# Optimization experiments

Hardware: AMD Instinct MI355X
Metric: run time of the kernel (lower is better)

The kernel has to match this reference:

```python
import jax, jax.numpy as jnp
import numpy as np

B, S, D_MODEL = 2, 2048, 2048
N_HEADS, N_KV_HEADS, HEAD_DIM = 32, 8, 64
N_GROUPS = N_HEADS // N_KV_HEADS


def setup_inputs() -> dict:
    key = jax.random.key(0)
    ks = jax.random.split(key, 5)
    x = jax.random.normal(ks[0], (B, S, D_MODEL), dtype=jnp.float32)
    wq = jax.random.normal(ks[1], (N_HEADS * HEAD_DIM, D_MODEL), dtype=jnp.float32) * 0.02
    wk = jax.random.normal(ks[2], (N_KV_HEADS * HEAD_DIM, D_MODEL), dtype=jnp.float32) * 0.02
    wv = jax.random.normal(ks[3], (N_KV_HEADS * HEAD_DIM, D_MODEL), dtype=jnp.float32) * 0.02
    wo = jax.random.normal(ks[4], (D_MODEL, N_HEADS * HEAD_DIM), dtype=jnp.float32) * 0.02
    # Rotary tables: module's apply_rope expects cos/sin of shape [S, head_dim//2]
    half = HEAD_DIM // 2
    inv_freq = 1.0 / (10000.0 ** (jnp.arange(0, half, dtype=jnp.float32) / half))
    angles = jnp.arange(S, dtype=jnp.float32)[:, None] * inv_freq[None, :]  # [S, half]
    cos = jnp.cos(angles)
    sin = jnp.sin(angles)
    return {"x": x, "wq": wq, "wk": wk, "wv": wv, "wo": wo, "cos": cos, "sin": sin}


def _rotate_half(t):
    half = t.shape[-1] // 2
    return jnp.concatenate((-t[..., half:], t[..., :half]), axis=-1)


def _apply_rope(q, k, cos, sin):
    # cos/sin: [S, head_dim//2] -> repeat_interleave(2) -> [S, head_dim]
    cos2 = jnp.repeat(cos, 2, axis=-1)[None, :, None, :]  # [1,S,1,D]
    sin2 = jnp.repeat(sin, 2, axis=-1)[None, :, None, :]
    q_rot = q * cos2 + _rotate_half(q) * sin2
    k_rot = k * cos2 + _rotate_half(k) * sin2
    return q_rot, k_rot


def reference(x, wq, wk, wv, wo, cos, sin):
    b, s, _ = x.shape
    q = (x @ wq.T).reshape(b, s, N_HEADS, HEAD_DIM)
    k = (x @ wk.T).reshape(b, s, N_KV_HEADS, HEAD_DIM)
    v = (x @ wv.T).reshape(b, s, N_KV_HEADS, HEAD_DIM)
    q, k = _apply_rope(q, k, cos, sin)
    # GQA expansion: repeat_interleave along head dim
    k = jnp.repeat(k, N_GROUPS, axis=2)  # [b,s,H,D]
    v = jnp.repeat(v, N_GROUPS, axis=2)
    q = q.transpose(0, 2, 1, 3)  # [b,H,s,D]
    k = k.transpose(0, 2, 1, 3)
    v = v.transpose(0, 2, 1, 3)
    scale = HEAD_DIM ** -0.5
    scores = jnp.einsum("bhqd,bhkd->bhqk", q, k) * scale
    causal = jnp.tril(jnp.ones((s, s), dtype=bool))
    scores = jnp.where(causal[None, None], scores, jnp.finfo(scores.dtype).min)
    attn = jax.nn.softmax(scores, axis=-1)
    out = jnp.einsum("bhqk,bhkd->bhqd", attn, v)
    out = out.transpose(0, 2, 1, 3).reshape(b, s, N_HEADS * HEAD_DIM)
    return out @ wo.T
```

## Files before the change

kernel.cpp:

```cpp
#include <hip/hip_runtime.h>
#include <hip/hip_bf16.h>

#define B_   2
#define S_   2048
#define DM   2048
#define NH   32
#define NKV  8
#define HD   64
#define MROWS 4096
#define NQKV  3072

typedef __attribute__((ext_vector_type(8))) short bf16x8;
typedef __attribute__((ext_vector_type(4))) float f32x4;
typedef __attribute__((ext_vector_type(16))) float f32x16;

__device__ __forceinline__ unsigned short f2b(float f) {
  __hip_bfloat16 h = __float2bfloat16(f);
  return *reinterpret_cast<unsigned short*>(&h);
}

__device__ __forceinline__ void gload16(const void* g, void* l) {
  __builtin_amdgcn_global_load_lds((__attribute__((address_space(1))) void*)g,
                                   (__attribute__((address_space(3))) void*)l,
                                   16, 0, 0);
// ... 87 lines not shown
  };
  auto ldB = [&](int buf, int row, int c16) -> bf16x8 {
    return *(const bf16x8*)((const char*)&Bbuf[buf][0] + row * 128 + ((c16 ^ (row & 7)) << 4));
  };

  f32x4 acc[4][4];
#pragma unroll
  for (int a = 0; a < 4; a++)
#pragma unroll
    for (int b2 = 0; b2 < 4; b2++) acc[a][b2] = (f32x4){0.f, 0.f, 0.f, 0.f};

  const int l15 = lane & 15, l4 = lane >> 4;

  stage_half(0, 0, 0); stage_half(0, 0, 1);
  stage_half(1, 64, 0); stage_half(1, 64, 1);
  asm volatile("s_waitcnt vmcnt(6)" ::: "memory");
  __builtin_amdgcn_s_barrier();

  int cur = 0;
  for (int t = 0; t < NT; ++t) {
    const int nxt2 = (cur >= 1) ? cur - 1 : cur + 2;
    {
      bf16x8 af[4], bfv[4];
#pragma unroll
      for (int mt = 0; mt < 4; ++mt) af[mt] = ldA(cur, wr * 64 + mt * 16 + l15, l4);
#pragma unroll
      for (int nt = 0; nt < 4; ++nt) bfv[nt] = ldB(cur, wc * 64 + nt * 16 + l15, l4);
      if (t + 2 < NT) stage_half(nxt2, (t + 2) * 64, 0);
      __builtin_amdgcn_s_barrier();
      __builtin_amdgcn_s_setprio(1);
#pragma unroll
      for (int mt = 0; mt < 4; ++mt)
#pragma unroll
        for (int nt = 0; nt < 4; ++nt)
          acc[mt][nt] = __builtin_amdgcn_mfma_f32_16x16x32_bf16(af[mt], bfv[nt], acc[mt][nt], 0, 0, 0);
      __builtin_amdgcn_s_setprio(0);
      __builtin_amdgcn_s_barrier();
    }
    {
      bf16x8 af[4], bfv[4];
#pragma unroll
      for (int mt = 0; mt < 4; ++mt) af[mt] = ldA(cur, wr * 64 + mt * 16 + l15, 4 + l4);
#pragma unroll
      for (int nt = 0; nt < 4; ++nt) bfv[nt] = ldB(cur, wc * 64 + nt * 16 + l15, 4 + l4);
      if (t + 2 < NT) stage_half(nxt2, (t + 2) * 64, 1);
      __builtin_amdgcn_s_barrier();
      __builtin_amdgcn_s_setprio(1);
#pragma unroll
      for (int mt = 0; mt < 4; ++mt)
#pragma unroll
        for (int nt = 0; nt < 4; ++nt)
          acc[mt][nt] = __builtin_amdgcn_mfma_f32_16x16x32_bf16(af[mt], bfv[nt], acc[mt][nt], 0, 0, 0);
      __builtin_amdgcn_s_setprio(0);
      if (t < NT - 1) {
        if (t + 2 < NT) asm volatile("s_waitcnt vmcnt(6)" ::: "memory");
        else            asm volatile("s_waitcnt vmcnt(0)" ::: "memory");
        __builtin_amdgcn_s_barrier();
      }
    }
    cur = (cur < 2) ? cur + 1 : 0;
  }

  const int orow = rowbase + wr * 64, ocol = colbase + wc * 64;
#pragma unroll
  for (int mt = 0; mt < 4; ++mt)
#pragma unroll
    for (int r = 0; r < 4; ++r) {
      const int row = orow + mt * 16 + l4 * 4 + r;
      const int s = row & 2047;
      const float* cR = cosg + s * 32;
      const float* sR = sing + s * 32;
#pragma unroll
      for (int nt = 0; nt < 2; ++nt) {
        const int i2 = nt * 8 + (l15 >> 1);
        float c0 = cR[i2], sv0 = sR[i2], c1 = cR[16 + i2], sv1 = sR[16 + i2];
        float alo = acc[mt][nt][r], ahi = acc[mt][nt + 2][r];
        size_t base = (size_t)row * 2048 + ocol + nt * 16 + l15;
        Qb[base]      = f2b((alo * c0 - ahi * sv0) * QSCALE);
        Qb[base + 32] = f2b((ahi * c1 + alo * sv1) * QSCALE);
      }
    }
}

__global__ __launch_bounds__(256, 3) void gemm_kv(const unsigned short* __restrict__ A,
                                                  const unsigned short* __restrict__ Bm,
                                                  unsigned short* __restrict__ Kb2,
                                                  unsigned short* __restrict__ Vtb,
                                                  const float* __restrict__ cosg,
                                                  const float* __restrict__ sing) {
  const int K = DM;
  __shared__ unsigned short Abuf[3][128 * 32];
  __shared__ unsigned short Bbuf[3][128 * 32];
  const int tid = threadIdx.x;
  const int wave = tid >> 6, lane = tid & 63;
  const int wr = wave >> 1, wc = wave & 1;
  const int rowbase = blockIdx.y * 128;
  const int colbase = blockIdx.x * 128;
  const unsigned short* Ag = A + (size_t)rowbase * K;
  const unsigned short* Bg = Bm + (size_t)colbase * K;
  const int NT = K / 32;

  auto stage = [&](int buf, int k0) {
#pragma unroll
    for (int it = 0; it < 2; ++it) {
      int slot = wave * 128 + it * 64 + lane;
      int r = slot >> 2, p = slot & 3;
      gload16(Ag + (size_t)r * K + k0 + ((p ^ ((r >> 1) & 3)) << 3),
              &Abuf[buf][(wave * 128 + it * 64) * 8]);
    }
#pragma unroll
    for (int it = 0; it < 2; ++it) {
      int slot = wave * 128 + it * 64 + lane;
      int r = slot >> 2, p = slot & 3;
      gload16(Bg + (size_t)r * K + k0 + ((p ^ ((r >> 1) & 3)) << 3),
              &Bbuf[buf][(wave * 128 + it * 64) * 8]);
    }
  };
  auto ldA = [&](int buf, int row, int c) -> bf16x8 {
    return *(const bf16x8*)((const char*)&Abuf[buf][0] + row * 64 + ((c ^ ((row >> 1) & 3)) << 4));
  };
  auto ldB = [&](int buf, int row, int c) -> bf16x8 {
    return *(const bf16x8*)((const char*)&Bbuf[buf][0] + row * 64 + ((c ^ ((row >> 1) & 3)) << 4));
  };

  f32x4 acc[4][4];
#pragma unroll
  for (int a = 0; a < 4; a++)
#pragma unroll
    for (int b2 = 0; b2 < 4; b2++) acc[a][b2] = (f32x4){0.f, 0.f, 0.f, 0.f};

  const int l15 = lane & 15, l4 = lane >> 4;

  stage(0, 0);
  stage(1, 32);
  asm volatile("s_waitcnt vmcnt(4)" ::: "memory");
  __builtin_amdgcn_s_barrier();

  int cur = 0;
  for (int t = 0; t < NT; ++t) {
    const int nxt2 = (cur >= 1) ? cur - 1 : cur + 2;
    bf16x8 af[4], bfv[4];
#pragma unroll
    for (int mt = 0; mt < 4; ++mt) af[mt] = ldA(cur, wr * 64 + mt * 16 + l15, l4);
#pragma unroll
    for (int nt = 0; nt < 4; ++nt) bfv[nt] = ldB(cur, wc * 64 + nt * 16 + l15, l4);
    if (t + 2 < NT) stage(nxt2, (t + 2) * 32);
    __builtin_amdgcn_s_barrier();
    __builtin_amdgcn_s_setprio(1);
#pragma unroll
    for (int mt = 0; mt < 4; ++mt)
#pragma unroll
      for (int nt = 0; nt < 4; ++nt)
        acc[mt][nt] = __builtin_amdgcn_mfma_f32_16x16x32_bf16(af[mt], bfv[nt], acc[mt][nt], 0, 0, 0);
    __builtin_amdgcn_s_setprio(0);
    if (t < NT - 1) {
      if (t + 2 < NT) asm volatile("s_waitcnt vmcnt(4)" ::: "memory");
      else            asm volatile("s_waitcnt vmcnt(0)" ::: "memory");
      __builtin_amdgcn_s_barrier();
    }
    cur = (cur < 2) ? cur + 1 : 0;
  }

  const int orow = rowbase + wr * 64, ocol = colbase + wc * 64;
  if (colbase < 512) {
#pragma unroll
    for (int mt = 0; mt < 4; ++mt)
#pragma unroll
      for (int r = 0; r < 4; ++r) {
        const int row = orow + mt * 16 + l4 * 4 + r;
        const int s = row & 2047;
        const float* cR = cosg + s * 32;
        const float* sR = sing + s * 32;
#pragma unroll
        for (int nt = 0; nt < 2; ++nt) {
          const int i2 = nt * 8 + (l15 >> 1);
          float c0 = cR[i2], sv0 = sR[i2], c1 = cR[16 + i2], sv1 = sR[16 + i2];
          float alo = acc[mt][nt][r], ahi = acc[mt][nt + 2][r];
          size_t base = (size_t)row * 512 + ocol + nt * 16 + l15;
          Kb2[base]      = f2b(alo * c0 - ahi * sv0);
          Kb2[base + 32] = f2b(ahi * c1 + alo * sv1);
        }
      }
  } else {
    const int hkv = (ocol - 512) >> 6;
#pragma unroll
    for (int mt = 0; mt < 4; ++mt)
#pragma unroll
      for (int nt = 0; nt < 4; ++nt) {
        const int d = nt * 16 + l15;
        const int row0 = orow + mt * 16 + l4 * 4;
        const int b = row0 >> 11, s0i = row0 & 2047;
        ushort4 u;
        u.x = f2b(acc[mt][nt][0]); u.y = f2b(acc[mt][nt][1]);
        u.z = f2b(acc[mt][nt][2]); u.w = f2b(acc[mt][nt][3]);
        *(ushort4*)(Vtb + ((size_t)(b * NKV + hkv) * HD + d) * S_ + s0i) = u;
      }
  }
}

#define BMg 256
#define BNg 128
#define BKg 64
__global__ __launch_bounds__(512, 2) void gemm_bt(const unsigned short* __restrict__ A,
                                                  const unsigned short* __restrict__ Bm,
                                                  float* __restrict__ C,
                                                  int M, int N, int K) {
  __shared__ unsigned short Abuf[3][BMg * BKg];
  __shared__ unsigned short Bbuf[3][BNg * BKg];
  const int tid = threadIdx.x;
  const int wave = tid >> 6, lane = tid & 63;
  const int wr = wave >> 1, wc = wave & 1;
  const int rowbase = blockIdx.y * BMg;
  const int colbase = blockIdx.x * BNg;
  const unsigned short* Ag = A + (size_t)rowbase * K;
  const unsigned short* Bg = Bm + (size_t)colbase * K;
  const int NT = K / BKg;

  auto stage_half = [&](int buf, int k0, int half) {
#pragma unroll
    for (int i = 0; i < 2; ++i) {
      int c = wave * 256 + (half * 2 + i) * 64 + lane;
      int r = c >> 3, p = c & 7;
      gload16(Ag + (size_t)r * K + k0 + ((p ^ (r & 7)) << 3),
              &Abuf[buf][(wave * 256 + (half * 2 + i) * 64) * 8]);
    }
    int c = wave * 128 + half * 64 + lane;
    int r = c >> 3, p = c & 7;
    gload16(Bg + (size_t)r * K + k0 + ((p ^ (r & 7)) << 3),
            &Bbuf[buf][(wave * 128 + half * 64) * 8]);
  };
  auto ldA = [&](int buf, int row, int c16) -> bf16x8 {
    return *(const bf16x8*)((const char*)&Abuf[buf][0] + row * 128 + ((c16 ^ (row & 7)) << 4));
  };
  auto ldB = [&](int buf, int row, int c16) -> bf16x8 {
    return *(const bf16x8*)((const char*)&Bbuf[buf][0] + row * 128 + ((c16 ^ (row & 7)) << 4));
  };

  f32x4 acc[4][4];
#pragma unroll
  for (int a = 0; a < 4; a++)
#pragma unroll
    for (int b2 = 0; b2 < 4; b2++) acc[a][b2] = (f32x4){0.f, 0.f, 0.f, 0.f};

  const int l15 = lane & 15, l4 = lane >> 4;

  stage_half(0, 0, 0); stage_half(0, 0, 1);
  stage_half(1, BKg, 0); stage_half(1, BKg, 1);
  asm volatile("s_waitcnt vmcnt(6)" ::: "memory");
  __builtin_amdgcn_s_barrier();

  int cur = 0;
  for (int t = 0; t < NT; ++t) {
    const int nxt2 = (cur >= 1) ? cur - 1 : cur + 2;
    {
      bf16x8 af[4], bfv[4];
#pragma unroll
      for (int mt = 0; mt < 4; ++mt) af[mt] = ldA(cur, wr * 64 + mt * 16 + l15, l4);
#pragma unroll
      for (int nt = 0; nt < 4; ++nt) bfv[nt] = ldB(cur, wc * 64 + nt * 16 + l15, l4);
      if (t + 2 < NT) stage_half(nxt2, (t + 2) * BKg, 0);
      __builtin_amdgcn_s_barrier();
      __builtin_amdgcn_s_setprio(1);
#pragma unroll
      for (int mt = 0; mt < 4; ++mt)
#pragma unroll
        for (int nt = 0; nt < 4; ++nt)
          acc[mt][nt] = __builtin_amdgcn_mfma_f32_16x16x32_bf16(af[mt], bfv[nt], acc[mt][nt], 0, 0, 0);
      __builtin_amdgcn_s_setprio(0);
      __builtin_amdgcn_s_barrier();
    }
    {
      bf16x8 af[4], bfv[4];
#pragma unroll
      for (int mt = 0; mt < 4; ++mt) af[mt] = ldA(cur, wr * 64 + mt * 16 + l15, 4 + l4);
#pragma unroll
      for (int nt = 0; nt < 4; ++nt) bfv[nt] = ldB(cur, wc * 64 + nt * 16 + l15, 4 + l4);
      if (t + 2 < NT) stage_half(nxt2, (t + 2) * BKg, 1);
      __builtin_amdgcn_s_barrier();
      __builtin_amdgcn_s_setprio(1);
#pragma unroll
      for (int mt = 0; mt < 4; ++mt)
#pragma unroll
        for (int nt = 0; nt < 4; ++nt)
          acc[mt][nt] = __builtin_amdgcn_mfma_f32_16x16x32_bf16(af[mt], bfv[nt], acc[mt][nt], 0, 0, 0);
      __builtin_amdgcn_s_setprio(0);
      if (t < NT - 1) {
        if (t + 2 < NT) asm volatile("s_waitcnt vmcnt(6)" ::: "memory");
        else            asm volatile("s_waitcnt vmcnt(0)" ::: "memory");
        __builtin_amdgcn_s_barrier();
      }
    }
    cur = (cur < 2) ? cur + 1 : 0;
  }

  const int orow = rowbase + wr * 64, ocol = colbase + wc * 64;
#pragma unroll
  for (int mt = 0; mt < 4; mt++)
#pragma unroll
    for (int nt = 0; nt < 4; nt++)
#pragma unroll
      for (int r = 0; r < 4; r++)
        C[(size_t)(orow + mt * 16 + l4 * 4 + r) * N + ocol + nt * 16 + l15] = acc[mt][nt][r];
}

__global__ __launch_bounds__(256, 2) void attn_kernel(const unsigned short* __restrict__ Qb,
                                                      const unsigned short* __restrict__ Kb2,
                                                      const unsigned short* __restrict__ Vt,
                                                      unsigned short* __restrict__ AO) {
  const int pr = blockIdx.x, h = blockIdx.y, b = blockIdx.z;
  const int hk = h >> 2;
  __shared__ unsigned short Kbuf[2][8192];
  __shared__ unsigned short Vbuf[2][8192];
  const int tid = threadIdx.x, wave = tid >> 6, lane = tid & 63;
  const int l31 = lane & 31, hi = lane >> 5;

  const unsigned short* Qrow = Qb + (size_t)b * S_ * 2048 + h * 64;
  const unsigned short* Krow = Kb2 + (size_t)b * S_ * 512 + hk * 64;
  const unsigned short* Vbase = Vt + (size_t)(b * NKV + hk) * HD * S_;

  const int NT_A = 16 - pr;
  const int NTtot = 17;

  auto j0_of = [&](int tl) { return (tl < NT_A ? tl : tl - NT_A) * 128; };
  auto stage = [&](int j0, int bufi) {
#pragma unroll
    for (int it = 0; it < 4; ++it) {
      int slot = (wave * 4 + it) * 64 + lane;
      int row = slot >> 3, p = slot & 7;
      gload16(Krow + (size_t)(j0 + row) * 512 + ((p ^ (row & 7)) << 3),
              &Kbuf[bufi][(wave * 4 + it) * 512]);
    }
#pragma unroll
    for (int it = 0; it < 4; ++it) {
      int slot = (wave * 4 + it) * 64 + lane;
      int row = slot >> 4, p = slot & 15;
      gload16(Vbase + (size_t)row * S_ + j0 + ((p ^ (row & 15)) << 3),
              &Vbuf[bufi][(wave * 4 + it) * 512]);
    }
  };

  stage(j0_of(0), 0);
  stage(j0_of(1), 1);
  asm volatile("s_waitcnt vmcnt(8)" ::: "memory");
  __builtin_amdgcn_s_barrier();

  int cur = 0, tlin = 0;

  for (int rg = 0; rg < 2; ++rg) {
    const int qbi = rg == 0 ? (15 - pr) : pr;
    const int qb = qbi * 128;
    const int NT = qbi + 1;
    const int q0w = qb + wave * 32;
    const int qg = q0w + l31;

    bf16x8 qf[4];
#pragma unroll
    for (int c = 0; c < 4; ++c)
      qf[c] = *reinterpret_cast<const bf16x8*>(Qrow + (size_t)qg * 2048 + c * 16 + hi * 8);

    f32x16 Oa0 = {}, Oa1 = {};
    float m_old = -INFINITY, lsum = 0.f;

    for (int t = 0; t < NT; ++t, ++tlin) {
      const int j0 = t * 128;

      if (j0 < q0w + 32) {
        const char* Klc = (const char*)&Kbuf[cur][0];
        const char* Vlc = (const char*)&Vbuf[cur][0];

        f32x16 s0 = {}, s1 = {}, s2 = {}, s3 = {};
        __builtin_amdgcn_s_setprio(1);
#pragma unroll
        for (int c = 0; c < 4; ++c) {
          const int xb = ((c << 1) + hi) ^ (l31 & 7);
          bf16x8 kf0 = *(const bf16x8*)(Klc + (l31) * 128       + (xb << 4));
          s0 = __builtin_amdgcn_mfma_f32_32x32x16_bf16(kf0, qf[c], s0, 0, 0, 0);
          bf16x8 kf1 = *(const bf16x8*)(Klc + (32 + l31) * 128  + (xb << 4));
          s1 = __builtin_amdgcn_mfma_f32_32x32x16_bf16(kf1, qf[c], s1, 0, 0, 0);
          bf16x8 kf2 = *(const bf16x8*)(Klc + (64 + l31) * 128  + (xb << 4));
          s2 = __builtin_amdgcn_mfma_f32_32x32x16_bf16(kf2, qf[c], s2, 0, 0, 0);
          bf16x8 kf3 = *(const bf16x8*)(Klc + (96 + l31) * 128  + (xb << 4));
          s3 = __builtin_amdgcn_mfma_f32_32x32x16_bf16(kf3, qf[c], s3, 0, 0, 0);
        }
        __builtin_amdgcn_s_setprio(0);

        if (j0 + 127 > q0w) {
          const int kb0 = j0 + 4 * hi, kb1 = kb0 + 32, kb2m = kb0 + 64, kb3 = kb0 + 96;
#pragma unroll
          for (int r = 0; r < 16; ++r) {
            const int ko = (r & 3) + 8 * (r >> 2);
            if (kb0 + ko > qg) s0[r] = -INFINITY;
            if (kb1 + ko > qg) s1[r] = -INFINITY;
            if (kb2m + ko > qg) s2[r] = -INFINITY;
            if (kb3 + ko > qg) s3[r] = -INFINITY;
          }
        }

        float a0 = fmaxf(fmaxf(s0[0], s1[0]), fmaxf(s2[0], s3[0]));
        float a1 = fmaxf(fmaxf(s0[1], s1[1]), fmaxf(s2[1], s3[1]));
        float a2 = fmaxf(fmaxf(s0[2], s1[2]), fmaxf(s2[2], s3[2]));
        float a3 = fmaxf(fmaxf(s0[3], s1[3]), fmaxf(s2[3], s3[3]));
#pragma unroll
        for (int r = 4; r < 16; r += 4) {
          a0 = fmaxf(a0, fmaxf(fmaxf(s0[r], s1[r]), fmaxf(s2[r], s3[r])));
          a1 = fmaxf(a1, fmaxf(fmaxf(s0[r + 1], s1[r + 1]), fmaxf(s2[r + 1], s3[r + 1])));
          a2 = fmaxf(a2, fmaxf(fmaxf(s0[r + 2], s1[r + 2]), fmaxf(s2[r + 2], s3[r + 2])));
          a3 = fmaxf(a3, fmaxf(fmaxf(s0[r + 3], s1[r + 3]), fmaxf(s2[r + 3], s3[r + 3])));
        }
        float mxt = fmaxf(fmaxf(a0, a1), fmaxf(a2, a3));
        mxt = fmaxf(mxt, __shfl_xor(mxt, 32, 64));

        if (!__all(mxt - m_old <= 8.f)) {
          float mnew = fmaxf(m_old, mxt);
          float corr = exp2hw(m_old - mnew);
          m_old = mnew;
          lsum *= corr;
#pragma unroll
          for (int r = 0; r < 16; ++r) { Oa0[r] *= corr; Oa1[r] *= corr; }
        }

        float t0 = 0.f, t1 = 0.f, t2 = 0.f, t3 = 0.f;
#pragma unroll
        for (int r = 0; r < 16; r += 4) {
          s0[r]     = exp2hw(s0[r] - m_old);     t0 += s0[r];
          s0[r + 1] = exp2hw(s0[r + 1] - m_old); t1 += s0[r + 1];
          s0[r + 2] = exp2hw(s0[r + 2] - m_old); t2 += s0[r + 2];
          s0[r + 3] = exp2hw(s0[r + 3] - m_old); t3 += s0[r + 3];
        }
#pragma unroll
        for (int r = 0; r < 16; r += 4) {
          s1[r]     = exp2hw(s1[r] - m_old);     t0 += s1[r];
          s1[r + 1] = exp2hw(s1[r + 1] - m_old); t1 += s1[r + 1];
          s1[r + 2] = exp2hw(s1[r + 2] - m_old); t2 += s1[r + 2];
          s1[r + 3] = exp2hw(s1[r + 3] - m_old); t3 += s1[r + 3];
        }
#pragma unroll
        for (int r = 0; r < 16; r += 4) {
          s2[r]     = exp2hw(s2[r] - m_old);     t0 += s2[r];
          s2[r + 1] = exp2hw(s2[r + 1] - m_old); t1 += s2[r + 1];
          s2[r + 2] = exp2hw(s2[r + 2] - m_old); t2 += s2[r + 2];
          s2[r + 3] = exp2hw(s2[r + 3] - m_old); t3 += s2[r + 3];
        }
#pragma unroll
        for (int r = 0; r < 16; r += 4) {
          s3[r]     = exp2hw(s3[r] - m_old);     t0 += s3[r];
          s3[r + 1] = exp2hw(s3[r + 1] - m_old); t1 += s3[r + 1];
          s3[r + 2] = exp2hw(s3[r + 2] - m_old); t2 += s3[r + 2];
          s3[r + 3] = exp2hw(s3[r + 3] - m_old); t3 += s3[r + 3];
        }
        float rs = (t0 + t1) + (t2 + t3);
        rs += __shfl_xor(rs, 32, 64);
        lsum += rs;

        bf16x8 pf0, pf1, pf2, pf3, pf4, pf5, pf6, pf7;
        {
          unsigned aA = cvtpk(s0[0], s0[1]),  bA = cvtpk(s0[4], s0[5]);  pl32swap(aA, bA);
          unsigned aB = cvtpk(s0[2], s0[3]),  bB = cvtpk(s0[6], s0[7]);  pl32swap(aB, bB);
          pf0 = mk8(aA, aB, bA, bB);
          unsigned aC = cvtpk(s0[8], s0[9]),  bC = cvtpk(s0[12], s0[13]); pl32swap(aC, bC);
          unsigned aD = cvtpk(s0[10], s0[11]), bD = cvtpk(s0[14], s0[15]); pl32swap(aD, bD);
          pf1 = mk8(aC, aD, bC, bD);
        }
        {
          unsigned aA = cvtpk(s1[0], s1[1]),  bA = cvtpk(s1[4], s1[5]);  pl32swap(aA, bA);
          unsigned aB = cvtpk(s1[2], s1[3]),  bB = cvtpk(s1[6], s1[7]);  pl32swap(aB, bB);
          pf2 = mk8(aA, aB, bA, bB);
          unsigned aC = cvtpk(s1[8], s1[9]),  bC = cvtpk(s1[12], s1[13]); pl32swap(aC, bC);
          unsigned aD = cvtpk(s1[10], s1[11]), bD = cvtpk(s1[14], s1[15]); pl32swap(aD, bD);
          pf3 = mk8(aC, aD, bC, bD);
        }
        {
          unsigned aA = cvtpk(s2[0], s2[1]),  bA = cvtpk(s2[4], s2[5]);  pl32swap(aA, bA);
          unsigned aB = cvtpk(s2[2], s2[3]),  bB = cvtpk(s2[6], s2[7]);  pl32swap(aB, bB);
          pf4 = mk8(aA, aB, bA, bB);
          unsigned aC = cvtpk(s2[8], s2[9]),  bC = cvtpk(s2[12], s2[13]); pl32swap(aC, bC);
          unsigned aD = cvtpk(s2[10], s2[11]), bD = cvtpk(s2[14], s2[15]); pl32swap(aD, bD);
          pf5 = mk8(aC, aD, bC, bD);
        }
        {
          unsigned aA = cvtpk(s3[0], s3[1]),  bA = cvtpk(s3[4], s3[5]);  pl32swap(aA, bA);
          unsigned aB = cvtpk(s3[2], s3[3]),  bB = cvtpk(s3[6], s3[7]);  pl32swap(aB, bB);
          pf6 = mk8(aA, aB, bA, bB);
          unsigned aC = cvtpk(s3[8], s3[9]),  bC = cvtpk(s3[12], s3[13]); pl32swap(aC, bC);
          unsigned aD = cvtpk(s3[10], s3[11]), bD = cvtpk(s3[14], s3[15]); pl32swap(aD, bD);
          pf7 = mk8(aC, aD, bC, bD);
        }

        const int xv = l31 & 15;
        __builtin_amdgcn_s_setprio(1);
#define PVSTEP(PF, SK)                                                                     \
        {                                                                                  \
          const int xc = (((SK) << 1) + hi) ^ xv;                                          \
          bf16x8 vf0 = *(const bf16x8*)(Vlc + l31 * 256 + (xc << 4));                      \
          Oa0 = __builtin_amdgcn_mfma_f32_32x32x16_bf16(vf0, PF, Oa0, 0, 0, 0);            \
          bf16x8 vf1 = *(const bf16x8*)(Vlc + (32 + l31) * 256 + (xc << 4));               \
          Oa1 = __builtin_amdgcn_mfma_f32_32x32x16_bf16(vf1, PF, Oa1, 0, 0, 0);            \
        }
        PVSTEP(pf0, 0) PVSTEP(pf1, 1) PVSTEP(pf2, 2) PVSTEP(pf3, 3)
        PVSTEP(pf4, 4) PVSTEP(pf5, 5) PVSTEP(pf6, 6) PVSTEP(pf7, 7)
#undef PVSTEP
        __builtin_amdgcn_s_setprio(0);
      }

      __builtin_amdgcn_s_barrier();
      if (tlin + 2 < NTtot) stage(j0_of(tlin + 2), cur);
      if (tlin + 1 < NTtot) {
        if (tlin + 2 < NTtot) asm volatile("s_waitcnt vmcnt(8)" ::: "memory");
        else                  asm volatile("s_waitcnt vmcnt(0)" ::: "memory");
        __builtin_amdgcn_s_barrier();
      }
      cur ^= 1;
    }

    const float inv = 1.0f / lsum;
    unsigned short* ob = AO + (size_t)(b * S_ + qg) * 2048 + h * 64;
#pragma unroll
    for (int c = 0; c < 4; ++c) {
      ushort4 u0, u1;
      u0.x = f2b(Oa0[4 * c] * inv);     u0.y = f2b(Oa0[4 * c + 1] * inv);
      u0.z = f2b(Oa0[4 * c + 2] * inv); u0.w = f2b(Oa0[4 * c + 3] * inv);
      u1.x = f2b(Oa1[4 * c] * inv);     u1.y = f2b(Oa1[4 * c + 1] * inv);
      u1.z = f2b(Oa1[4 * c + 2] * inv); u1.w = f2b(Oa1[4 * c + 3] * inv);
      *(ushort4*)(ob + 8 * c + 4 * hi)      = u0;
      *(ushort4*)(ob + 32 + 8 * c + 4 * hi) = u1;
    }
  }
}

extern "C" void kernel_launch(void* const* d_in, const int* in_sizes, int n_in,
                              void* d_out, int out_size, void* d_ws, size_t ws_size,
                              hipStream_t stream) {
  (void)in_sizes; (void)n_in; (void)out_size; (void)ws_size;
  const float* x    = (const float*)d_in[0];
  const float* wq   = (const float*)d_in[1];
  const float* wk   = (const float*)d_in[2];
  const float* wv   = (const float*)d_in[3];
  const float* wo   = (const float*)d_in[4];
  const float* cosg = (const float*)d_in[5];
  const float* sing = (const float*)d_in[6];

  char* ws = (char*)d_ws;
  unsigned short* xb   = (unsigned short*)(ws);
  unsigned short* wcat = (unsigned short*)(ws + 16777216);
  unsigned short* wob  = (unsigned short*)(ws + 29360128);
  unsigned short* Qb   = (unsigned short*)(ws + 37748736);
  unsigned short* Kb2  = (unsigned short*)(ws + 54525952);
  unsigned short* Vtb  = (unsigned short*)(ws + 58720256);
  unsigned short* AO   = xb;

  f2bf_kernel<<<8192, 256, 0, stream>>>(x, xb, 2097152);
  wcat_kernel<<<6144, 256, 0, stream>>>(wq, wk, wv, wcat);
  f2bf_kernel<<<4096, 256, 0, stream>>>(wo, wob, 1048576);

  gemm_q<<<dim3(DM / 128, MROWS / 256), 512, 0, stream>>>(xb, wcat, Qb, cosg, sing);
  gemm_kv<<<dim3(1024 / 128, MROWS / 128), 256, 0, stream>>>(xb, wcat + (size_t)2048 * 2048,
                                                             Kb2, Vtb, cosg, sing);

  attn_kernel<<<dim3(8, NH, B_), 256, 0, stream>>>(Qb, Kb2, Vtb, AO);

  gemm_bt<<<dim3(DM / BNg, MROWS / BMg), 512, 0, stream>>>(AO, wob, (float*)d_out, MROWS, DM, DM);
}
```

Measured before the change: 190.6 us.

## Retile KV GEMM and restructure attention to one query block per workgroup with register prefetch

The K/V projection GEMM now uses 128x64 tiles with BK=64, one wave per 32 rows, and a wider XOR swizzle. This doubles the grid so more workgroups fill the GPU. The attention kernel drops the paired-query-block scheme with async global-to-LDS double buffering. Each workgroup now handles a single query block, with a 1D grid remapped to interleave causal workloads, register-staged prefetch of the next K/V tile, and a single LDS buffer. The smaller LDS footprint allows 4 blocks per CU for higher occupancy, at the cost of the direct-to-LDS loads, extra barriers, and less even per-block work.

```diff
diff --git a/kernel.cpp b/kernel.cpp
--- a/kernel.cpp
+++ b/kernel.cpp
@@ -193,89 +193,90 @@
     }
 }
 
-__global__ __launch_bounds__(256, 3) void gemm_kv(const unsigned short* __restrict__ A,
+__global__ __launch_bounds__(256, 2) void gemm_kv(const unsigned short* __restrict__ A,
                                                   const unsigned short* __restrict__ Bm,
                                                   unsigned short* __restrict__ Kb2,
                                                   unsigned short* __restrict__ Vtb,
                                                   const float* __restrict__ cosg,
                                                   const float* __restrict__ sing) {
   const int K = DM;
-  __shared__ unsigned short Abuf[3][128 * 32];
-  __shared__ unsigned short Bbuf[3][128 * 32];
+  __shared__ unsigned short Abuf[3][128 * 64];
+  __shared__ unsigned short Bbuf[3][64 * 64];
   const int tid = threadIdx.x;
   const int wave = tid >> 6, lane = tid & 63;
-  const int wr = wave >> 1, wc = wave & 1;
   const int rowbase = blockIdx.y * 128;
-  const int colbase = blockIdx.x * 128;
+  const int colbase = blockIdx.x * 64;
   const unsigned short* Ag = A + (size_t)rowbase * K;
   const unsigned short* Bg = Bm + (size_t)colbase * K;
-  const int NT = K / 32;
+  const int NT = K / 64;
 
   auto stage = [&](int buf, int k0) {
 #pragma unroll
+    for (int it = 0; it < 4; ++it) {
+      int s = (wave * 4 + it) * 64 + lane;
+      int r = s >> 3, p = s & 7;
+      gload16(Ag + (size_t)r * K + k0 + ((p ^ (r & 7)) << 3),
+              &Abuf[buf][((wave * 4 + it) * 64) * 8]);
+    }
+#pragma unroll
     for (int it = 0; it < 2; ++it) {
-      int slot = wave * 128 + it * 64 + lane;
-      int r = slot >> 2, p = slot & 3;
-      gload16(Ag + (size_t)r * K + k0 + ((p ^ ((r >> 1) & 3)) << 3),
-              &Abuf[buf][(wave * 128 + it * 64) * 8]);
-    }
-#pragma unroll
-    for (int it = 0; it < 2; ++it) {
-      int slot = wave * 128 + it * 64 + lane;
-      int r = slot >> 2, p = slot & 3;
-      gload16(Bg + (size_t)r * K + k0 + ((p ^ ((r >> 1) & 3)) << 3),
-              &Bbuf[buf][(wave * 128 + it * 64) * 8]);
-    }
-  };
-  auto ldA = [&](int buf, int row, int c) -> bf16x8 {
-    return *(const bf16x8*)((const char*)&Abuf[buf][0] + row * 64 + ((c ^ ((row >> 1) & 3)) << 4));
-  };
-  auto ldB = [&](int buf, int row, int c) -> bf16x8 {
-    return *(const bf16x8*)((const char*)&Bbuf[buf][0] + row * 64 + ((c ^ ((row >> 1) & 3)) << 4));
-  };
-
-  f32x4 acc[4][4];
-#pragma unroll
-  for (int a = 0; a < 4; a++)
+      int s = (wave * 2 + it) * 64 + lane;
+      int r = s >> 3, p = s & 7;
+      gload16(Bg + (size_t)r * K + k0 + ((p ^ (r & 7)) << 3),
+              &Bbuf[buf][((wave * 2 + it) * 64) * 8]);
+    }
+  };
+  auto ldA = [&](int buf, int row, int c16) -> bf16x8 {
+    return *(const bf16x8*)((const char*)&Abuf[buf][0] + row * 128 + ((c16 ^ (row & 7)) << 4));
+  };
+  auto ldB = [&](int buf, int row, int c16) -> bf16x8 {
+    return *(const bf16x8*)((const char*)&Bbuf[buf][0] + row * 128 + ((c16 ^ (row & 7)) << 4));
+  };
+
+  f32x4 acc[2][4];
+#pragma unroll
+  for (int a = 0; a < 2; a++)
 #pragma unroll
     for (int b2 = 0; b2 < 4; b2++) acc[a][b2] = (f32x4){0.f, 0.f, 0.f, 0.f};
 
   const int l15 = lane & 15, l4 = lane >> 4;
 
   stage(0, 0);
-  stage(1, 32);
-  asm volatile("s_waitcnt vmcnt(4)" ::: "memory");
+  stage(1, 64);
+  asm volatile("s_waitcnt vmcnt(6)" ::: "memory");
   __builtin_amdgcn_s_barrier();
 
   int cur = 0;
   for (int t = 0; t < NT; ++t) {
     const int nxt2 = (cur >= 1) ? cur - 1 : cur + 2;
-    bf16x8 af[4], bfv[4];
-#pragma unroll
-    for (int mt = 0; mt < 4; ++mt) af[mt] = ldA(cur, wr * 64 + mt * 16 + l15, l4);
-#pragma unroll
-    for (int nt = 0; nt < 4; ++nt) bfv[nt] = ldB(cur, wc * 64 + nt * 16 + l15, l4);
-    if (t + 2 < NT) stage(nxt2, (t + 2) * 32);
-    __builtin_amdgcn_s_barrier();
-    __builtin_amdgcn_s_setprio(1);
-#pragma unroll
-    for (int mt = 0; mt < 4; ++mt)
-#pragma unroll
-      for (int nt = 0; nt < 4; ++nt)
-        acc[mt][nt] = __builtin_amdgcn_mfma_f32_16x16x32_bf16(af[mt], bfv[nt], acc[mt][nt], 0, 0, 0);
-    __builtin_amdgcn_s_setprio(0);
+#pragma unroll
+    for (int ph = 0; ph < 2; ++ph) {
+      bf16x8 af[2], bfv[4];
+#pragma unroll
+      for (int mt = 0; mt < 2; ++mt) af[mt] = ldA(cur, wave * 32 + mt * 16 + l15, ph * 4 + l4);
+#pragma unroll
+      for (int nt = 0; nt < 4; ++nt) bfv[nt] = ldB(cur, nt * 16 + l15, ph * 4 + l4);
+      if (ph == 0 && t + 2 < NT) stage(nxt2, (t + 2) * 64);
+      __builtin_amdgcn_s_setprio(1);
+#pragma unroll
+      for (int mt = 0; mt < 2; ++mt)
+#pragma unroll
+        for (int nt = 0; nt < 4; ++nt)
+          acc[mt][nt] = __builtin_amdgcn_mfma_f32_16x16x32_bf16(af[mt], bfv[nt], acc[mt][nt], 0, 0, 0);
+      __builtin_amdgcn_s_setprio(0);
+    }
     if (t < NT - 1) {
-      if (t + 2 < NT) asm volatile("s_waitcnt vmcnt(4)" ::: "memory");
+      if (t + 2 < NT) asm volatile("s_waitcnt vmcnt(6)" ::: "memory");
       else            asm volatile("s_waitcnt vmcnt(0)" ::: "memory");
       __builtin_amdgcn_s_barrier();
     }
     cur = (cur < 2) ? cur + 1 : 0;
   }
 
-  const int orow = rowbase + wr * 64, ocol = colbase + wc * 64;
+  const int orow = rowbase + wave * 32;
   if (colbase < 512) {
 #pragma unroll
-    for (int mt = 0; mt < 4; ++mt)
+    for (int mt = 0; mt < 2; ++mt)
 #pragma unroll
       for (int r = 0; r < 4; ++r) {
         const int row = orow + mt * 16 + l4 * 4 + r;
@@ -287,15 +288,15 @@
           const int i2 = nt * 8 + (l15 >> 1);
           float c0 = cR[i2], sv0 = sR[i2], c1 = cR[16 + i2], sv1 = sR[16 + i2];
           float alo = acc[mt][nt][r], ahi = acc[mt][nt + 2][r];
-          size_t base = (size_t)row * 512 + ocol + nt * 16 + l15;
+          size_t base = (size_t)row * 512 + colbase + nt * 16 + l15;
           Kb2[base]      = f2b(alo * c0 - ahi * sv0);
           Kb2[base + 32] = f2b(ahi * c1 + alo * sv1);
         }
       }
   } else {
-    const int hkv = (ocol - 512) >> 6;
-#pragma unroll
-    for (int mt = 0; mt < 4; ++mt)
+    const int hkv = (colbase - 512) >> 6;
+#pragma unroll
+    for (int mt = 0; mt < 2; ++mt)
 #pragma unroll
       for (int nt = 0; nt < 4; ++nt) {
         const int d = nt * 16 + l15;
@@ -414,14 +415,25 @@
         C[(size_t)(orow + mt * 16 + l4 * 4 + r) * N + ocol + nt * 16 + l15] = acc[mt][nt][r];
 }
 
-__global__ __launch_bounds__(256, 2) void attn_kernel(const unsigned short* __restrict__ Qb,
+__global__ __launch_bounds__(256, 4) void attn_kernel(const unsigned short* __restrict__ Qb,
                                                       const unsigned short* __restrict__ Kb2,
                                                       const unsigned short* __restrict__ Vt,
                                                       unsigned short* __restrict__ AO) {
-  const int pr = blockIdx.x, h = blockIdx.y, b = blockIdx.z;
+  const int jid = blockIdx.x;
+  const int hi4 = jid >> 8;
+  const int lo  = jid & 255;
+  const int a   = lo & 15;
+  int qbi;
+  if      (hi4 == 0) qbi = a;
+  else if (hi4 == 1) qbi = 15 - a;
+  else if (hi4 == 2) qbi = (a + 8) & 15;
+  else               qbi = (7 - a) & 15;
+  const int bh = (lo >> 4) * 4 + hi4;
+  const int h = bh & 31, b = bh >> 5;
   const int hk = h >> 2;
-  __shared__ unsigned short Kbuf[2][8192];
-  __shared__ unsigned short Vbuf[2][8192];
+
+  __shared__ unsigned short Kl[128 * 64];
+  __shared__ unsigned short Vl[64 * 128];
   const int tid = threadIdx.x, wave = tid >> 6, lane = tid & 63;
   const int l31 = lane & 31, hi = lane >> 5;
 
@@ -429,212 +441,218 @@
   const unsigned short* Krow = Kb2 + (size_t)b * S_ * 512 + hk * 64;
   const unsigned short* Vbase = Vt + (size_t)(b * NKV + hk) * HD * S_;
 
-  const int NT_A = 16 - pr;
-  const int NTtot = 17;
-
-  auto j0_of = [&](int tl) { return (tl < NT_A ? tl : tl - NT_A) * 128; };
-  auto stage = [&](int j0, int bufi) {
+  const int NT = qbi + 1;
+  const int qb = qbi * 128;
+  const int q0w = qb + wave * 32;
+  const int qg = q0w + l31;
+
+  int krow[4], kc[4], vrow[4], vc[4];
+#pragma unroll
+  for (int it = 0; it < 4; ++it) {
+    int s = (wave * 4 + it) * 64 + lane;
+    krow[it] = s >> 3;  kc[it] = s & 7;
+    vrow[it] = s >> 4;  vc[it] = s & 15;
+  }
+
+  auto write_lds = [&](const uint4* kr, const uint4* vr) {
 #pragma unroll
     for (int it = 0; it < 4; ++it) {
-      int slot = (wave * 4 + it) * 64 + lane;
-      int row = slot >> 3, p = slot & 7;
-      gload16(Krow + (size_t)(j0 + row) * 512 + ((p ^ (row & 7)) << 3),
-              &Kbuf[bufi][(wave * 4 + it) * 512]);
-    }
+      *(uint4*)((char*)Kl + krow[it] * 128 + ((kc[it] ^ (krow[it] & 7)) << 4)) = kr[it];
+      *(uint4*)((char*)Vl + vrow[it] * 256 + ((vc[it] ^ (vrow[it] & 15)) << 4)) = vr[it];
+    }
+  };
+
+  {
+    uint4 kr[4], vr[4];
 #pragma unroll
     for (int it = 0; it < 4; ++it) {
-      int slot = (wave * 4 + it) * 64 + lane;
-      int row = slot >> 4, p = slot & 15;
-      gload16(Vbase + (size_t)row * S_ + j0 + ((p ^ (row & 15)) << 3),
-              &Vbuf[bufi][(wave * 4 + it) * 512]);
-    }
-  };
-
-  stage(j0_of(0), 0);
-  stage(j0_of(1), 1);
-  asm volatile("s_waitcnt vmcnt(8)" ::: "memory");
-  __builtin_amdgcn_s_barrier();
-
-  int cur = 0, tlin = 0;
-
-  for (int rg = 0; rg < 2; ++rg) {
-    const int qbi = rg == 0 ? (15 - pr) : pr;
-    const int qb = qbi * 128;
-    const int NT = qbi + 1;
-    const int q0w = qb + wave * 32;
-    const int qg = q0w + l31;
-
-    bf16x8 qf[4];
-#pragma unroll
-    for (int c = 0; c < 4; ++c)
-      qf[c] = *reinterpret_cast<const bf16x8*>(Qrow + (size_t)qg * 2048 + c * 16 + hi * 8);
-
-    f32x16 Oa0 = {}, Oa1 = {};
-    float m_old = -INFINITY, lsum = 0.f;
-
-    for (int t = 0; t < NT; ++t, ++tlin) {
-      const int j0 = t * 128;
-
-      if (j0 < q0w + 32) {
-        const char* Klc = (const char*)&Kbuf[cur][0];
-        const char* Vlc = (const char*)&Vbuf[cur][0];
-
-        f32x16 s0 = {}, s1 = {}, s2 = {}, s3 = {};
-        __builtin_amdgcn_s_setprio(1);
-#pragma unroll
-        for (int c = 0; c < 4; ++c) {
-          const int xb = ((c << 1) + hi) ^ (l31 & 7);
-          bf16x8 kf0 = *(const bf16x8*)(Klc + (l31) * 128       + (xb << 4));
-          s0 = __builtin_amdgcn_mfma_f32_32x32x16_bf16(kf0, qf[c], s0, 0, 0, 0);
-          bf16x8 kf1 = *(const bf16x8*)(Klc + (32 + l31) * 128  + (xb << 4));
-          s1 = __builtin_amdgcn_mfma_f32_32x32x16_bf16(kf1, qf[c], s1, 0, 0, 0);
-          bf16x8 kf2 = *(const bf16x8*)(Klc + (64 + l31) * 128  + (xb << 4));
-          s2 = __builtin_amdgcn_mfma_f32_32x32x16_bf16(kf2, qf[c], s2, 0, 0, 0);
-          bf16x8 kf3 = *(const bf16x8*)(Klc + (96 + l31) * 128  + (xb << 4));
-          s3 = __builtin_amdgcn_mfma_f32_32x32x16_bf16(kf3, qf[c], s3, 0, 0, 0);
+      kr[it] = *(const uint4*)(Krow + (size_t)krow[it] * 512 + kc[it] * 8);
+      vr[it] = *(const uint4*)(Vbase + (size_t)vrow[it] * S_ + vc[it] * 8);
+    }
+    write_lds(kr, vr);
+    asm volatile("s_waitcnt lgkmcnt(0)" ::: "memory");
+    __builtin_amdgcn_s_barrier();
+  }
+
+  bf16x8 qf[4];
+#pragma unroll
+  for (int c = 0; c < 4; ++c)
+    qf[c] = *reinterpret_cast<const bf16x8*>(Qrow + (size_t)qg * 2048 + c * 16 + hi * 8);
+
+  f32x16 Oa0 = {}, Oa1 = {};
+  float m_old = -INFINITY, lsum = 0.f;
+
+  for (int t = 0; t < NT; ++t) {
+    const int j0 = t * 128;
+
+    uint4 kr[4], vr[4];
+    const bool more = (t + 1 < NT);
+    if (more) {
+      const int j0n = j0 + 128;
+#pragma unroll
+      for (int it = 0; it < 4; ++it) {
+        kr[it] = *(const uint4*)(Krow + (size_t)(j0n + krow[it]) * 512 + kc[it] * 8);
+        vr[it] = *(const uint4*)(Vbase + (size_t)vrow[it] * S_ + j0n + vc[it] * 8);
+      }
+    }
+
+    {
+      const char* Klc = (const char*)Kl;
+      const char* Vlc = (const char*)Vl;
+
+      f32x16 s0 = {}, s1 = {}, s2 = {}, s3 = {};
+      __builtin_amdgcn_s_setprio(1);
+#pragma unroll
+      for (int c = 0; c < 4; ++c) {
+        const int xb = ((c << 1) + hi) ^ (l31 & 7);
+        bf16x8 kf0 = *(const bf16x8*)(Klc + (l31) * 128       + (xb << 4));
+        s0 = __builtin_amdgcn_mfma_f32_32x32x16_bf16(kf0, qf[c], s0, 0, 0, 0);
+        bf16x8 kf1 = *(const bf16x8*)(Klc + (32 + l31) * 128  + (xb << 4));
+        s1 = __builtin_amdgcn_mfma_f32_32x32x16_bf16(kf1, qf[c], s1, 0, 0, 0);
+        bf16x8 kf2 = *(const bf16x8*)(Klc + (64 + l31) * 128  + (xb << 4));
+        s2 = __builtin_amdgcn_mfma_f32_32x32x16_bf16(kf2, qf[c], s2, 0, 0, 0);
+        bf16x8 kf3 = *(const bf16x8*)(Klc + (96 + l31) * 128  + (xb << 4));
+        s3 = __builtin_amdgcn_mfma_f32_32x32x16_bf16(kf3, qf[c], s3, 0, 0, 0);
+      }
+      __builtin_amdgcn_s_setprio(0);
+
+      if (j0 + 127 > q0w) {
+        const int kb0 = j0 + 4 * hi, kb1 = kb0 + 32, kb2m = kb0 + 64, kb3 = kb0 + 96;
+#pragma unroll
+        for (int r = 0; r < 16; ++r) {
+          const int ko = (r & 3) + 8 * (r >> 2);
+          if (kb0 + ko > qg) s0[r] = -INFINITY;
+          if (kb1 + ko > qg) s1[r] = -INFINITY;
+          if (kb2m + ko > qg) s2[r] = -INFINITY;
+          if (kb3 + ko > qg) s3[r] = -INFINITY;
         }
-        __builtin_amdgcn_s_setprio(0);
-
-        if (j0 + 127 > q0w) {
-          const int kb0 = j0 + 4 * hi, kb1 = kb0 + 32, kb2m = kb0 + 64, kb3 = kb0 + 96;
-#pragma unroll
-          for (int r = 0; r < 16; ++r) {
-            const int ko = (r & 3) + 8 * (r >> 2);
-            if (kb0 + ko > qg) s0[r] = -INFINITY;
-            if (kb1 + ko > qg) s1[r] = -INFINITY;
-            if (kb2m + ko > qg) s2[r] = -INFINITY;
-            if (kb3 + ko > qg) s3[r] = -INFINITY;
-          }
-        }
-
-        float a0 = fmaxf(fmaxf(s0[0], s1[0]), fmaxf(s2[0], s3[0]));
-        float a1 = fmaxf(fmaxf(s0[1], s1[1]), fmaxf(s2[1], s3[1]));
-        float a2 = fmaxf(fmaxf(s0[2], s1[2]), fmaxf(s2[2], s3[2]));
-        float a3 = fmaxf(fmaxf(s0[3], s1[3]), fmaxf(s2[3], s3[3]));
-#pragma unroll
-        for (int r = 4; r < 16; r += 4) {
-          a0 = fmaxf(a0, fmaxf(fmaxf(s0[r], s1[r]), fmaxf(s2[r], s3[r])));
-          a1 = fmaxf(a1, fmaxf(fmaxf(s0[r + 1], s1[r + 1]), fmaxf(s2[r + 1], s3[r + 1])));
-          a2 = fmaxf(a2, fmaxf(fmaxf(s0[r + 2], s1[r + 2]), fmaxf(s2[r + 2], s3[r + 2])));
-          a3 = fmaxf(a3, fmaxf(fmaxf(s0[r + 3], s1[r + 3]), fmaxf(s2[r + 3], s3[r + 3])));
-        }
-        float mxt = fmaxf(fmaxf(a0, a1), fmaxf(a2, a3));
-        mxt = fmaxf(mxt, __shfl_xor(mxt, 32, 64));
-
-        if (!__all(mxt - m_old <= 8.f)) {
-          float mnew = fmaxf(m_old, mxt);
-          float corr = exp2hw(m_old - mnew);
-          m_old = mnew;
-          lsum *= corr;
-#pragma unroll
-          for (int r = 0; r < 16; ++r) { Oa0[r] *= corr; Oa1[r] *= corr; }
-        }
-
-        float t0 = 0.f, t1 = 0.f, t2 = 0.f, t3 = 0.f;
-#pragma unroll
-        for (int r = 0; r < 16; r += 4) {
-          s0[r]     = exp2hw(s0[r] - m_old);     t0 += s0[r];
-          s0[r + 1] = exp2hw(s0[r + 1] - m_old); t1 += s0[r + 1];
-          s0[r + 2] = exp2hw(s0[r + 2] - m_old); t2 += s0[r + 2];
-          s0[r + 3] = exp2hw(s0[r + 3] - m_old); t3 += s0[r + 3];
-        }
-#pragma unroll
-        for (int r = 0; r < 16; r += 4) {
-          s1[r]     = exp2hw(s1[r] - m_old);     t0 += s1[r];
-          s1[r + 1] = exp2hw(s1[r + 1] - m_old); t1 += s1[r + 1];
-          s1[r + 2] = exp2hw(s1[r + 2] - m_old); t2 += s1[r + 2];
-          s1[r + 3] = exp2hw(s1[r + 3] - m_old); t3 += s1[r + 3];
-        }
-#pragma unroll
-        for (int r = 0; r < 16; r += 4) {
-          s2[r]     = exp2hw(s2[r] - m_old);     t0 += s2[r];
-          s2[r + 1] = exp2hw(s2[r + 1] - m_old); t1 += s2[r + 1];
-          s2[r + 2] = exp2hw(s2[r + 2] - m_old); t2 += s2[r + 2];
-          s2[r + 3] = exp2hw(s2[r + 3] - m_old); t3 += s2[r + 3];
-        }
-#pragma unroll
-        for (int r = 0; r < 16; r += 4) {
-          s3[r]     = exp2hw(s3[r] - m_old);     t0 += s3[r];
-          s3[r + 1] = exp2hw(s3[r + 1] - m_old); t1 += s3[r + 1];
-          s3[r + 2] = exp2hw(s3[r + 2] - m_old); t2 += s3[r + 2];
-          s3[r + 3] = exp2hw(s3[r + 3] - m_old); t3 += s3[r + 3];
-        }
-        float rs = (t0 + t1) + (t2 + t3);
-        rs += __shfl_xor(rs, 32, 64);
-        lsum += rs;
-
-        bf16x8 pf0, pf1, pf2, pf3, pf4, pf5, pf6, pf7;
-        {
-          unsigned aA = cvtpk(s0[0], s0[1]),  bA = cvtpk(s0[4], s0[5]);  pl32swap(aA, bA);
-          unsigned aB = cvtpk(s0[2], s0[3]),  bB = cvtpk(s0[6], s0[7]);  pl32swap(aB, bB);
-          pf0 = mk8(aA, aB, bA, bB);
-          unsigned aC = cvtpk(s0[8], s0[9]),  bC = cvtpk(s0[12], s0[13]); pl32swap(aC, bC);
-          unsigned aD = cvtpk(s0[10], s0[11]), bD = cvtpk(s0[14], s0[15]); pl32swap(aD, bD);
-          pf1 = mk8(aC, aD, bC, bD);
-        }
-        {
-          unsigned aA = cvtpk(s1[0], s1[1]),  bA = cvtpk(s1[4], s1[5]);  pl32swap(aA, bA);
-          unsigned aB = cvtpk(s1[2], s1[3]),  bB = cvtpk(s1[6], s1[7]);  pl32swap(aB, bB);
-          pf2 = mk8(aA, aB, bA, bB);
-          unsigned aC = cvtpk(s1[8], s1[9]),  bC = cvtpk(s1[12], s1[13]); pl32swap(aC, bC);
-          unsigned aD = cvtpk(s1[10], s1[11]), bD = cvtpk(s1[14], s1[15]); pl32swap(aD, bD);
-          pf3 = mk8(aC, aD, bC, bD);
-        }
-        {
-          unsigned aA = cvtpk(s2[0], s2[1]),  bA = cvtpk(s2[4], s2[5]);  pl32swap(aA, bA);
-          unsigned aB = cvtpk(s2[2], s2[3]),  bB = cvtpk(s2[6], s2[7]);  pl32swap(aB, bB);
-          pf4 = mk8(aA, aB, bA, bB);
-          unsigned aC = cvtpk(s2[8], s2[9]),  bC = cvtpk(s2[12], s2[13]); pl32swap(aC, bC);
-          unsigned aD = cvtpk(s2[10], s2[11]), bD = cvtpk(s2[14], s2[15]); pl32swap(aD, bD);
-          pf5 = mk8(aC, aD, bC, bD);
-        }
-        {
-          unsigned aA = cvtpk(s3[0], s3[1]),  bA = cvtpk(s3[4], s3[5]);  pl32swap(aA, bA);
-          unsigned aB = cvtpk(s3[2], s3[3]),  bB = cvtpk(s3[6], s3[7]);  pl32swap(aB, bB);
-          pf6 = mk8(aA, aB, bA, bB);
-          unsigned aC = cvtpk(s3[8], s3[9]),  bC = cvtpk(s3[12], s3[13]); pl32swap(aC, bC);
-          unsigned aD = cvtpk(s3[10], s3[11]), bD = cvtpk(s3[14], s3[15]); pl32swap(aD, bD);
-          pf7 = mk8(aC, aD, bC, bD);
-        }
-
-        const int xv = l31 & 15;
-        __builtin_amdgcn_s_setprio(1);
+      }
+
+      float a0 = fmaxf(fmaxf(s0[0], s1[0]), fmaxf(s2[0], s3[0]));
+      float a1 = fmaxf(fmaxf(s0[1], s1[1]), fmaxf(s2[1], s3[1]));
+      float a2 = fmaxf(fmaxf(s0[2], s1[2]), fmaxf(s2[2], s3[2]));
+      float a3 = fmaxf(fmaxf(s0[3], s1[3]), fmaxf(s2[3], s3[3]));
+#pragma unroll
+      for (int r = 4; r < 16; r += 4) {
+        a0 = fmaxf(a0, fmaxf(fmaxf(s0[r], s1[r]), fmaxf(s2[r], s3[r])));
+        a1 = fmaxf(a1, fmaxf(fmaxf(s0[r + 1], s1[r + 1]), fmaxf(s2[r + 1], s3[r + 1])));
+        a2 = fmaxf(a2, fmaxf(fmaxf(s0[r + 2], s1[r + 2]), fmaxf(s2[r + 2], s3[r + 2])));
+        a3 = fmaxf(a3, fmaxf(fmaxf(s0[r + 3], s1[r + 3]), fmaxf(s2[r + 3], s3[r + 3])));
+      }
+      float mxt = fmaxf(fmaxf(a0, a1), fmaxf(a2, a3));
+      mxt = fmaxf(mxt, __shfl_xor(mxt, 32, 64));
+
+      if (!__all(mxt - m_old <= 8.f)) {
+        float mnew = fmaxf(m_old, mxt);
+        float corr = exp2hw(m_old - mnew);
+        m_old = mnew;
+        lsum *= corr;
+#pragma unroll
+        for (int r = 0; r < 16; ++r) { Oa0[r] *= corr; Oa1[r] *= corr; }
+      }
+
+      float t0 = 0.f, t1 = 0.f, t2 = 0.f, t3 = 0.f;
+#pragma unroll
+      for (int r = 0; r < 16; r += 4) {
+        s0[r]     = exp2hw(s0[r] - m_old);     t0 += s0[r];
+        s0[r + 1] = exp2hw(s0[r + 1] - m_old); t1 += s0[r + 1];
+        s0[r + 2] = exp2hw(s0[r + 2] - m_old); t2 += s0[r + 2];
+        s0[r + 3] = exp2hw(s0[r + 3] - m_old); t3 += s0[r + 3];
+      }
+#pragma unroll
+      for (int r = 0; r < 16; r += 4) {
+        s1[r]     = exp2hw(s1[r] - m_old);     t0 += s1[r];
+        s1[r + 1] = exp2hw(s1[r + 1] - m_old); t1 += s1[r + 1];
+        s1[r + 2] = exp2hw(s1[r + 2] - m_old); t2 += s1[r + 2];
+        s1[r + 3] = exp2hw(s1[r + 3] - m_old); t3 += s1[r + 3];
+      }
+#pragma unroll
+      for (int r = 0; r < 16; r += 4) {
+        s2[r]     = exp2hw(s2[r] - m_old);     t0 += s2[r];
+        s2[r + 1] = exp2hw(s2[r + 1] - m_old); t1 += s2[r + 1];
+        s2[r + 2] = exp2hw(s2[r + 2] - m_old); t2 += s2[r + 2];
+        s2[r + 3] = exp2hw(s2[r + 3] - m_old); t3 += s2[r + 3];
+      }
+#pragma unroll
+      for (int r = 0; r < 16; r += 4) {
+        s3[r]     = exp2hw(s3[r] - m_old);     t0 += s3[r];
+        s3[r + 1] = exp2hw(s3[r + 1] - m_old); t1 += s3[r + 1];
+        s3[r + 2] = exp2hw(s3[r + 2] - m_old); t2 += s3[r + 2];
+        s3[r + 3] = exp2hw(s3[r + 3] - m_old); t3 += s3[r + 3];
+      }
+      float rs = (t0 + t1) + (t2 + t3);
+      rs += __shfl_xor(rs, 32, 64);
+      lsum += rs;
+
+      bf16x8 pf0, pf1, pf2, pf3, pf4, pf5, pf6, pf7;
+      {
+        unsigned aA = cvtpk(s0[0], s0[1]),  bA = cvtpk(s0[4], s0[5]);  pl32swap(aA, bA);
+        unsigned aB = cvtpk(s0[2], s0[3]),  bB = cvtpk(s0[6], s0[7]);  pl32swap(aB, bB);
+        pf0 = mk8(aA, aB, bA, bB);
+        unsigned aC = cvtpk(s0[8], s0[9]),  bC = cvtpk(s0[12], s0[13]); pl32swap(aC, bC);
+        unsigned aD = cvtpk(s0[10], s0[11]), bD = cvtpk(s0[14], s0[15]); pl32swap(aD, bD);
+        pf1 = mk8(aC, aD, bC, bD);
+      }
+      {
+        unsigned aA = cvtpk(s1[0], s1[1]),  bA = cvtpk(s1[4], s1[5]);  pl32swap(aA, bA);
+        unsigned aB = cvtpk(s1[2], s1[3]),  bB = cvtpk(s1[6], s1[7]);  pl32swap(aB, bB);
+        pf2 = mk8(aA, aB, bA, bB);
+        unsigned aC = cvtpk(s1[8], s1[9]),  bC = cvtpk(s1[12], s1[13]); pl32swap(aC, bC);
+        unsigned aD = cvtpk(s1[10], s1[11]), bD = cvtpk(s1[14], s1[15]); pl32swap(aD, bD);
+        pf3 = mk8(aC, aD, bC, bD);
+      }
+      {
+        unsigned aA = cvtpk(s2[0], s2[1]),  bA = cvtpk(s2[4], s2[5]);  pl32swap(aA, bA);
+        unsigned aB = cvtpk(s2[2], s2[3]),  bB = cvtpk(s2[6], s2[7]);  pl32swap(aB, bB);
+        pf4 = mk8(aA, aB, bA, bB);
+        unsigned aC = cvtpk(s2[8], s2[9]),  bC = cvtpk(s2[12], s2[13]); pl32swap(aC, bC);
+        unsigned aD = cvtpk(s2[10], s2[11]), bD = cvtpk(s2[14], s2[15]); pl32swap(aD, bD);
+        pf5 = mk8(aC, aD, bC, bD);
+      }
+      {
+        unsigned aA = cvtpk(s3[0], s3[1]),  bA = cvtpk(s3[4], s3[5]);  pl32swap(aA, bA);
+        unsigned aB = cvtpk(s3[2], s3[3]),  bB = cvtpk(s3[6], s3[7]);  pl32swap(aB, bB);
+        pf6 = mk8(aA, aB, bA, bB);
+        unsigned aC = cvtpk(s3[8], s3[9]),  bC = cvtpk(s3[12], s3[13]); pl32swap(aC, bC);
+        unsigned aD = cvtpk(s3[10], s3[11]), bD = cvtpk(s3[14], s3[15]); pl32swap(aD, bD);
+        pf7 = mk8(aC, aD, bC, bD);
+      }
+
+      const int xv = l31 & 15;
+      __builtin_amdgcn_s_setprio(1);
 #define PVSTEP(PF, SK)                                                                     \
-        {                                                                                  \
-          const int xc = (((SK) << 1) + hi) ^ xv;                                          \
-          bf16x8 vf0 = *(const bf16x8*)(Vlc + l31 * 256 + (xc << 4));                      \
-          Oa0 = __builtin_amdgcn_mfma_f32_32x32x16_bf16(vf0, PF, Oa0, 0, 0, 0);            \
-          bf16x8 vf1 = *(const bf16x8*)(Vlc + (32 + l31) * 256 + (xc << 4));               \
-          Oa1 = __builtin_amdgcn_mfma_f32_32x32x16_bf16(vf1, PF, Oa1, 0, 0, 0);            \
-        }
-        PVSTEP(pf0, 0) PVSTEP(pf1, 1) PVSTEP(pf2, 2) PVSTEP(pf3, 3)
-        PVSTEP(pf4, 4) PVSTEP(pf5, 5) PVSTEP(pf6, 6) PVSTEP(pf7, 7)
+      {                                                                                    \
+        const int xc = (((SK) << 1) + hi) ^ xv;                                            \
+        bf16x8 vf0 = *(const bf16x8*)(Vlc + l31 * 256 + (xc << 4));                        \
+        Oa0 = __builtin_amdgcn_mfma_f32_32x32x16_bf16(vf0, PF, Oa0, 0, 0, 0);              \
+        bf16x8 vf1 = *(const bf16x8*)(Vlc + (32 + l31) * 256 + (xc << 4));                 \
+        Oa1 = __builtin_amdgcn_mfma_f32_32x32x16_bf16(vf1, PF, Oa1, 0, 0, 0);              \
+      }
+      PVSTEP(pf0, 0) PVSTEP(pf1, 1) PVSTEP(pf2, 2) PVSTEP(pf3, 3)
+      PVSTEP(pf4, 4) PVSTEP(pf5, 5) PVSTEP(pf6, 6) PVSTEP(pf7, 7)
 #undef PVSTEP
-        __builtin_amdgcn_s_setprio(0);
-      }
-
-      __builtin_amdgcn_s_barrier();
-      if (tlin + 2 < NTtot) stage(j0_of(tlin + 2), cur);
-      if (tlin + 1 < NTtot) {
-        if (tlin + 2 < NTtot) asm volatile("s_waitcnt vmcnt(8)" ::: "memory");
-        else                  asm volatile("s_waitcnt vmcnt(0)" ::: "memory");
-        __builtin_amdgcn_s_barrier();
-      }
-      cur ^= 1;
-    }
-
-    const float inv = 1.0f / lsum;
-    unsigned short* ob = AO + (size_t)(b * S_ + qg) * 2048 + h * 64;
-#pragma unroll
-    for (int c = 0; c < 4; ++c) {
-      ushort4 u0, u1;
-      u0.x = f2b(Oa0[4 * c] * inv);     u0.y = f2b(Oa0[4 * c + 1] * inv);
-      u0.z = f2b(Oa0[4 * c + 2] * inv); u0.w = f2b(Oa0[4 * c + 3] * inv);
-      u1.x = f2b(Oa1[4 * c] * inv);     u1.y = f2b(Oa1[4 * c + 1] * inv);
-      u1.z = f2b(Oa1[4 * c + 2] * inv); u1.w = f2b(Oa1[4 * c + 3] * inv);
-      *(ushort4*)(ob + 8 * c + 4 * hi)      = u0;
-      *(ushort4*)(ob + 32 + 8 * c + 4 * hi) = u1;
-    }
+      __builtin_amdgcn_s_setprio(0);
+    }
+
+    if (more) {
+      __builtin_amdgcn_s_barrier();
+      write_lds(kr, vr);
+      asm volatile("s_waitcnt lgkmcnt(0)" ::: "memory");
+      __builtin_amdgcn_s_barrier();
+    }
+  }
+
+  const float inv = 1.0f / lsum;
+  unsigned short* ob = AO + (size_t)(b * S_ + qg) * 2048 + h * 64;
+#pragma unroll
+  for (int c = 0; c < 4; ++c) {
+    ushort4 u0, u1;
+    u0.x = f2b(Oa0[4 * c] * inv);     u0.y = f2b(Oa0[4 * c + 1] * inv);
+    u0.z = f2b(Oa0[4 * c + 2] * inv); u0.w = f2b(Oa0[4 * c + 3] * inv);
+    u1.x = f2b(Oa1[4 * c] * inv);     u1.y = f2b(Oa1[4 * c + 1] * inv);
+    u1.z = f2b(Oa1[4 * c + 2] * inv); u1.w = f2b(Oa1[4 * c + 3] * inv);
+    *(ushort4*)(ob + 8 * c + 4 * hi)      = u0;
+    *(ushort4*)(ob + 32 + 8 * c + 4 * hi) = u1;
   }
 }
 
@@ -664,10 +682,10 @@
   f2bf_kernel<<<4096, 256, 0, stream>>>(wo, wob, 1048576);
 
   gemm_q<<<dim3(DM / 128, MROWS / 256), 512, 0, stream>>>(xb, wcat, Qb, cosg, sing);
-  gemm_kv<<<dim3(1024 / 128, MROWS / 128), 256, 0, stream>>>(xb, wcat + (size_t)2048 * 2048,
-                                                             Kb2, Vtb, cosg, sing);
-
-  attn_kernel<<<dim3(8, NH, B_), 256, 0, stream>>>(Qb, Kb2, Vtb, AO);
+  gemm_kv<<<dim3(1024 / 64, MROWS / 128), 256, 0, stream>>>(xb, wcat + (size_t)2048 * 2048,
+                                                            Kb2, Vtb, cosg, sing);
+
+  attn_kernel<<<dim3(1024), 256, 0, stream>>>(Qb, Kb2, Vtb, AO);
 
   gemm_bt<<<dim3(DM / BNg, MROWS / BMg), 512, 0, stream>>>(AO, wob, (float*)d_out, MROWS, DM, DM);
 }
```

Result: slower. 319.5 us (+67.6%).
